# Kernel tuning notes

Measured on AMD Instinct MI355X. Metric: run time of the kernel, lower is better.

The kernel has to match this reference:

```python
import jax, jax.numpy as jnp
import numpy as np
import math

EMB_DIM = 1024
HEAD_SIZE = 64
T = 4096
B = 4

def setup_inputs() -> dict:
    key = jax.random.key(0)
    k1, k2, k3, k4 = jax.random.split(key, 4)
    scale = 1.0 / math.sqrt(EMB_DIM)
    return {
        "input": jax.random.normal(k1, (B, T, EMB_DIM), dtype=jnp.float32),
        "Wq": jax.random.normal(k2, (EMB_DIM, HEAD_SIZE), dtype=jnp.float32) * scale,
        "Wk": jax.random.normal(k3, (EMB_DIM, HEAD_SIZE), dtype=jnp.float32) * scale,
        "Wv": jax.random.normal(k4, (EMB_DIM, HEAD_SIZE), dtype=jnp.float32) * scale,
    }

def reference(input, Wq, Wk, Wv):
    # q,k,v: [B,T,H]
    q = input @ Wq
    k = input @ Wk
    v = input @ Wv
    # scores: [B,T,T]
    match = jnp.einsum('bqh,bkh->bqk', q, k)
    # 'encoder' mask in this repo = causal tril mask
    causal = jnp.tril(jnp.ones((T, T), dtype=bool))
    match = jnp.where(causal, match, -jnp.inf)
    # NOTE: faithful to source quirk: softmax first, THEN divide by sqrt(head_size)
    attention = jax.nn.softmax(match, axis=-1) / math.sqrt(HEAD_SIZE)
    return jnp.einsum('bqk,bkh->bqh', attention, v)
```

## Files before the change

### kernel.cpp

```cpp
#include <hip/hip_runtime.h>

#define T_SEQ 4096
#define NBATCH 4
#define EMB 1024
#define HS 64
#define BT (NBATCH * T_SEQ)

typedef float f32x4 __attribute__((ext_vector_type(4)));
typedef short s16x8 __attribute__((ext_vector_type(8)));

__device__ __forceinline__ unsigned short f2bf(float x) {
  union { float f; unsigned u; } c; c.f = x;
  unsigned r = c.u + 0x7FFF + ((c.u >> 16) & 1);
  return (unsigned short)(r >> 16);
}
__device__ __forceinline__ float bf2f(unsigned short h) {
  union { unsigned u; float f; } c; c.u = ((unsigned)h) << 16;
  return c.f;
}
__device__ __forceinline__ void cvt8(float4 a0, float4 a1, s16x8& hi, s16x8& lo) {
  float xv[8] = {a0.x, a0.y, a0.z, a0.w, a1.x, a1.y, a1.z, a1.w};
#pragma unroll
  for (int j = 0; j < 8; ++j) {
    unsigned short h = f2bf(xv[j]);
    hi[j] = (short)h;
    lo[j] = (short)f2bf(xv[j] - bf2f(h));
  }
}

__global__ __launch_bounds__(256) void wconv(
    const float* __restrict__ Wq, const float* __restrict__ Wk,
    const float* __restrict__ Wv, unsigned short* __restrict__ wt_hi,
    unsigned short* __restrict__ wt_lo) {
  const int n3 = blockIdx.x;
  const int which = n3 >> 6, n = n3 & 63;
  const float* W = (which == 0) ? Wq : (which == 1) ? Wk : Wv;
#pragma unroll
  for (int i = 0; i < 4; ++i) {
    int k = i * 256 + threadIdx.x;
    float x = W[(size_t)k * HS + n];
    unsigned short h = f2bf(x);
    wt_hi[(size_t)n3 * EMB + k] = h;
    wt_lo[(size_t)n3 * EMB + k] = f2bf(x - bf2f(h));
  }
}

__global__ __launch_bounds__(512) void qkv_mfma(
    const float* __restrict__ inp, const unsigned short* __restrict__ wt_hi,
    const unsigned short* __restrict__ wt_lo, float* __restrict__ qf,
    unsigned short* __restrict__ khi, unsigned short* __restrict__ klo,
    unsigned short* __restrict__ vtb) {
  __shared__ unsigned short Bhi[192 * 40];
  __shared__ unsigned short Blo[192 * 40];
  const int t = threadIdx.x, lane = t & 63, w = t >> 6;
  const int m = lane & 15, quad = lane >> 4;
  const int mg = w >> 2, ng = w & 3;
  const int tok0 = blockIdx.x * 32;
  const int arow = tok0 + mg * 16 + m;

  f32x4 acc[3];
#pragma unroll
  for (int nt = 0; nt < 3; ++nt) acc[nt] = (f32x4){0.f, 0.f, 0.f, 0.f};

  const size_t offa = (size_t)(t >> 2) * EMB + (t & 3) * 8;
  const int idxb = (t < 256) ? (t + 512) : (t - 256);
  const unsigned short* srcb = (t < 256) ? wt_hi : wt_lo;
  const size_t offb = (size_t)(idxb >> 2) * EMB + (idxb & 3) * 8;
  const int idxc = t + 256;
  const size_t offc = (size_t)(idxc >> 2) * EMB + (idxc & 3) * 8;

  uint4 bpa, bpb, bpc;
  float4 apre0, apre1;
  bpa = *(const uint4*)&wt_hi[offa];
  bpb = *(const uint4*)&srcb[offb];
  bpc = *(const uint4*)&wt_lo[offc];
  {
    const float* ap = &inp[(size_t)arow * EMB + quad * 8];
    apre0 = *(const float4*)ap;
    apre1 = *(const float4*)(ap + 4);
  }

  for (int kc = 0; kc < 32; ++kc) {
    const int k0n = (kc + 1) * 32;
    __syncthreads();
    {
      *(uint4*)&Bhi[(t >> 2) * 40 + (t & 3) * 8] = bpa;
      unsigned short* dstb = (t < 256) ? Bhi : Blo;
      *(uint4*)&dstb[(idxb >> 2) * 40 + (idxb & 3) * 8] = bpb;
      *(uint4*)&Blo[(idxc >> 2) * 40 + (idxc & 3) * 8] = bpc;
    }
    __syncthreads();

    s16x8 ah, al;
    cvt8(apre0, apre1, ah, al);

    if (kc < 31) {
      bpa = *(const uint4*)&wt_hi[offa + k0n];
      bpb = *(const uint4*)&srcb[offb + k0n];
      bpc = *(const uint4*)&wt_lo[offc + k0n];
      const float* ap = &inp[(size_t)arow * EMB + k0n + quad * 8];
      apre0 = *(const float4*)ap;
      apre1 = *(const float4*)(ap + 4);
    }

#pragma unroll
    for (int nt = 0; nt < 3; ++nt) {
      int n3 = ng * 48 + nt * 16 + m;
      s16x8 bh = *(const s16x8*)&Bhi[n3 * 40 + quad * 8];
      s16x8 bl = *(const s16x8*)&Blo[n3 * 40 + quad * 8];
      acc[nt] = __builtin_amdgcn_mfma_f32_16x16x32_bf16(ah, bh, acc[nt], 0, 0, 0);
      acc[nt] = __builtin_amdgcn_mfma_f32_16x16x32_bf16(ah, bl, acc[nt], 0, 0, 0);
      acc[nt] = __builtin_amdgcn_mfma_f32_16x16x32_bf16(al, bh, acc[nt], 0, 0, 0);
    }
  }

#pragma unroll
  for (int nt = 0; nt < 3; ++nt) {
    int n3 = ng * 48 + nt * 16 + m;
    int which = n3 >> 6, col = n3 & 63;
#pragma unroll
    for (int r = 0; r < 4; ++r) {
      int tok = tok0 + mg * 16 + quad * 4 + r;
      float val = acc[nt][r];
      if (which == 0) {
        qf[(size_t)tok * HS + col] = val;
      } else if (which == 1) {
        unsigned short h = f2bf(val);
        khi[(size_t)tok * HS + col] = h;
        klo[(size_t)tok * HS + col] = f2bf(val - bf2f(h));
      } else {
        vtb[(size_t)(tok >> 6) * 4096 + (size_t)col * 64 + (tok & 63)] = f2bf(val);
      }
    }
  }
}

__global__ __launch_bounds__(256) void attn_part(
    const float* __restrict__ q, const unsigned short* __restrict__ khi,
    const unsigned short* __restrict__ klo, const unsigned short* __restrict__ vt,
    unsigned short* __restrict__ partO, float* __restrict__ partML) {
  __shared__ unsigned short Khi_s[64 * 72];
  __shared__ unsigned short Klo_s[64 * 72];
  __shared__ unsigned short Vt_s[64 * 72];
  __shared__ unsigned short P_s[4 * 16 * 72];
  const int t = threadIdx.x;
  const int lane = t & 63, w = t >> 6;
  const int m = lane & 15, quad = lane >> 4;

  int u = blockIdx.x;
  const int b = u / 160;
  u -= b * 160;
  int qtile = 0, c = 0;
  {
    int acc2 = 0;
    for (int qq = 0; qq < 64; ++qq) {
      int ncq = (qq >> 4) + 1;
      if (u < acc2 + ncq) { qtile = qq; c = u - acc2; break; }
      acc2 += ncq;
    }
  }
  const int kt0 = c * 16;
  const int kt1 = (kt0 + 16 < qtile + 1) ? kt0 + 16 : qtile + 1;

  const size_t qrow0 = (size_t)b * T_SEQ + (size_t)qtile * 64;
  const size_t krowbase = (size_t)b * T_SEQ;
  const int q_loc = w * 16 + m;

  s16x8 qh[2], ql[2];
#pragma unroll
  for (int cc = 0; cc < 2; ++cc) {
    const float* qp = &q[(qrow0 + q_loc) * HS + cc * 32 + quad * 8];
    cvt8(*(const float4*)qp, *(const float4*)(qp + 4), qh[cc], ql[cc]);
  }

  float l_st = 0.f;
  f32x4 o[4];
#pragma unroll
  for (int hb = 0; hb < 4; ++hb) o[hb] = (f32x4){0.f, 0.f, 0.f, 0.f};

  const int r0 = t >> 3, ch0 = t & 7;
  const int r1 = (256 + t) >> 3, ch1 = t & 7;

  uint4 pk0h, pk0l, pv0, pk1h, pk1l, pv1;
  {
    size_t g0 = (krowbase + (size_t)kt0 * 64 + r0) * HS + ch0 * 8;
    size_t g1 = (krowbase + (size_t)kt0 * 64 + r1) * HS + ch1 * 8;
    pk0h = *(const uint4*)&khi[g0]; pk0l = *(const uint4*)&klo[g0];
    pk1h = *(const uint4*)&khi[g1]; pk1l = *(const uint4*)&klo[g1];
    size_t v0 = (size_t)(b * 64 + kt0) * 4096 + (size_t)r0 * 64 + ch0 * 8;
    size_t v1 = (size_t)(b * 64 + kt0) * 4096 + (size_t)r1 * 64 + ch1 * 8;
    pv0 = *(const uint4*)&vt[v0]; pv1 = *(const uint4*)&vt[v1];
  }

  for (int kt = kt0; kt < kt1; ++kt) {
    __syncthreads();
    *(uint4*)&Khi_s[r0 * 72 + ch0 * 8] = pk0h;
    *(uint4*)&Klo_s[r0 * 72 + ch0 * 8] = pk0l;
    *(uint4*)&Vt_s[r0 * 72 + ch0 * 8] = pv0;
    *(uint4*)&Khi_s[r1 * 72 + ch1 * 8] = pk1h;
    *(uint4*)&Klo_s[r1 * 72 + ch1 * 8] = pk1l;
    *(uint4*)&Vt_s[r1 * 72 + ch1 * 8] = pv1;
    __syncthreads();

    if (kt + 1 < kt1) {
      size_t g0 = (krowbase + (size_t)(kt + 1) * 64 + r0) * HS + ch0 * 8;
      size_t g1 = (krowbase + (size_t)(kt + 1) * 64 + r1) * HS + ch1 * 8;
      pk0h = *(const uint4*)&khi[g0]; pk0l = *(const uint4*)&klo[g0];
      pk1h = *(const uint4*)&khi[g1]; pk1l = *(const uint4*)&klo[g1];
      size_t v0 = (size_t)(b * 64 + kt + 1) * 4096 + (size_t)r0 * 64 + ch0 * 8;
      size_t v1 = (size_t)(b * 64 + kt + 1) * 4096 + (size_t)r1 * 64 + ch1 * 8;
      pv0 = *(const uint4*)&vt[v0]; pv1 = *(const uint4*)&vt[v1];
    }

    f32x4 st[4];
#pragma unroll
    for (int cb = 0; cb < 4; ++cb) {
      st[cb] = (f32x4){0.f, 0.f, 0.f, 0.f};
#pragma unroll
      for (int cc = 0; cc < 2; ++cc) {
        s16x8 bh = *(const s16x8*)&Khi_s[(cb * 16 + m) * 72 + cc * 32 + quad * 8];
        s16x8 bl = *(const s16x8*)&Klo_s[(cb * 16 + m) * 72 + cc * 32 + quad * 8];
        st[cb] = __builtin_amdgcn_mfma_f32_16x16x32_bf16(bh, qh[cc], st[cb], 0, 0, 0);
        st[cb] = __builtin_amdgcn_mfma_f32_16x16x32_bf16(bl, qh[cc], st[cb], 0, 0, 0);
        st[cb] = __builtin_amdgcn_mfma_f32_16x16x32_bf16(bh, ql[cc], st[cb], 0, 0, 0);
      }
    }
    if (kt == qtile) {
#pragma unroll
      for (int cb = 0; cb < 4; ++cb)
#pragma unroll
        for (int r = 0; r < 4; ++r)
          if (cb * 16 + quad * 4 + r > q_loc) st[cb][r] = -1e30f;
    }
#pragma unroll
    for (int cb = 0; cb < 4; ++cb)
#pragma unroll
      for (int r = 0; r < 4; ++r) {
        st[cb][r] = __expf(st[cb][r]);
        l_st += st[cb][r];
      }
#pragma unroll
    for (int cb = 0; cb < 4; ++cb) {
      uint2 pk;
      pk.x = (unsigned)f2bf(st[cb][0]) | ((unsigned)f2bf(st[cb][1]) << 16);
      pk.y = (unsigned)f2bf(st[cb][2]) | ((unsigned)f2bf(st[cb][3]) << 16);
      *(uint2*)&P_s[q_loc * 72 + cb * 16 + quad * 4] = pk;
    }
    s16x8 pf[2];
#pragma unroll
    for (int cc = 0; cc < 2; ++cc)
      pf[cc] = *(const s16x8*)&P_s[q_loc * 72 + cc * 32 + quad * 8];
#pragma unroll
    for (int hb = 0; hb < 4; ++hb) {
#pragma unroll
      for (int cc = 0; cc < 2; ++cc) {
        s16x8 vf = *(const s16x8*)&Vt_s[(hb * 16 + m) * 72 + cc * 32 + quad * 8];
        o[hb] = __builtin_amdgcn_mfma_f32_16x16x32_bf16(vf, pf[cc], o[hb], 0, 0, 0);
      }
    }
  }

  l_st += __shfl_xor(l_st, 16, 64);
  l_st += __shfl_xor(l_st, 32, 64);

  const int slot = ((b * 64 + qtile) << 2) + c;
  unsigned short* Op = partO + (size_t)slot * 4096;
#pragma unroll
  for (int hb = 0; hb < 4; ++hb) {
    uint2 pk;
    pk.x = (unsigned)f2bf(o[hb][0]) | ((unsigned)f2bf(o[hb][1]) << 16);
    pk.y = (unsigned)f2bf(o[hb][2]) | ((unsigned)f2bf(o[hb][3]) << 16);
    *(uint2*)&Op[q_loc * 64 + hb * 16 + quad * 4] = pk;
  }
  if (quad == 0) partML[(size_t)slot * 64 + q_loc] = l_st;
}

__global__ __launch_bounds__(256) void attn_combine(
    const unsigned short* __restrict__ partO, const float* __restrict__ partML,
    float* __restrict__ out) {
  const int qtile = blockIdx.x, b = blockIdx.y;
  const int t = threadIdx.x;
  const int row = t >> 2, hg = t & 3;
  const int nc = (qtile >> 4) + 1;
  const int slot0 = (b * 64 + qtile) << 2;

  float lsum = 0.f;
  for (int i = 0; i < nc; ++i) lsum += partML[(size_t)(slot0 + i) * 64 + row];
  const float inv = 1.f / (lsum * 8.0f);

  float acc[16];
#pragma unroll
  for (int e = 0; e < 16; ++e) acc[e] = 0.f;
  for (int i = 0; i < nc; ++i) {
    const unsigned short* Op =
        partO + (size_t)(slot0 + i) * 4096 + row * 64 + hg * 16;
    uint4 u0 = *(const uint4*)Op;
    uint4 u1 = *(const uint4*)(Op + 8);
    unsigned uv[8] = {u0.x, u0.y, u0.z, u0.w, u1.x, u1.y, u1.z, u1.w};
#pragma unroll
    for (int e = 0; e < 8; ++e) {
      acc[2 * e] += bf2f((unsigned short)(uv[e] & 0xFFFF));
      acc[2 * e + 1] += bf2f((unsigned short)(uv[e] >> 16));
    }
  }
  float* op = &out[((size_t)b * T_SEQ + (size_t)qtile * 64 + row) * HS + hg * 16];
#pragma unroll
  for (int v = 0; v < 4; ++v) {
    float4 r;
    r.x = acc[4 * v + 0] * inv; r.y = acc[4 * v + 1] * inv;
    r.z = acc[4 * v + 2] * inv; r.w = acc[4 * v + 3] * inv;
    ((float4*)op)[v] = r;
  }
}

extern "C" void kernel_launch(void* const* d_in, const int* in_sizes, int n_in,
                              void* d_out, int out_size, void* d_ws, size_t ws_size,
                              hipStream_t stream) {
  const float* inp = (const float*)d_in[0];
  const float* Wq  = (const float*)d_in[1];
  const float* Wk  = (const float*)d_in[2];
  const float* Wv  = (const float*)d_in[3];
  float* out = (float*)d_out;

  char* base = (char*)d_ws;
  float* qf = (float*)base;
  unsigned short* khi = (unsigned short*)(base + (size_t)BT * HS * 4);
  unsigned short* klo = khi + (size_t)BT * HS;
  unsigned short* vtb = klo + (size_t)BT * HS;
  unsigned short* wt_hi = vtb + (size_t)BT * HS;
  unsigned short* wt_lo = wt_hi + (size_t)192 * EMB;
  unsigned short* partO = wt_lo + (size_t)192 * EMB;
  float* partML = (float*)(partO + (size_t)1024 * 4096);

  wconv<<<dim3(192), dim3(256), 0, stream>>>(Wq, Wk, Wv, wt_hi, wt_lo);
  qkv_mfma<<<dim3(BT / 32), dim3(512), 0, stream>>>(inp, wt_hi, wt_lo, qf, khi, klo, vtb);
  attn_part<<<dim3(640), dim3(256), 0, stream>>>(qf, khi, klo, vtb, partO, partML);
  attn_combine<<<dim3(64, NBATCH), dim3(256), 0, stream>>>(partO, partML, out);
}
```

Baseline: 192.3 us.

## Enlarge QKV projection tile to 64 tokens and 64-wide K chunks

The QKV projection GEMM now processes 64 tokens per block instead of 32, with each warp computing six 16-column tiles instead of three, and walks K in chunks of 64 instead of 32. This halves the number of blocks and K-loop iterations, which cuts barrier count and how often each block reloads the shared weight tiles per token. In exchange it uses more registers per thread, more LDS per block, and launches fewer blocks (256), which may leave some CUs idle.

```diff
diff --git a/kernel.cpp b/kernel.cpp
--- a/kernel.cpp
+++ b/kernel.cpp
@@ -50,73 +50,93 @@
     const unsigned short* __restrict__ wt_lo, float* __restrict__ qf,
     unsigned short* __restrict__ khi, unsigned short* __restrict__ klo,
     unsigned short* __restrict__ vtb) {
-  __shared__ unsigned short Bhi[192 * 40];
-  __shared__ unsigned short Blo[192 * 40];
+  __shared__ unsigned short Bhi[192 * 72];
+  __shared__ unsigned short Blo[192 * 72];
   const int t = threadIdx.x, lane = t & 63, w = t >> 6;
   const int m = lane & 15, quad = lane >> 4;
-  const int mg = w >> 2, ng = w & 3;
-  const int tok0 = blockIdx.x * 32;
+  const int mg = w >> 1, ng = w & 1;
+  const int tok0 = blockIdx.x * 64;
   const int arow = tok0 + mg * 16 + m;
 
-  f32x4 acc[3];
-#pragma unroll
-  for (int nt = 0; nt < 3; ++nt) acc[nt] = (f32x4){0.f, 0.f, 0.f, 0.f};
-
-  const size_t offa = (size_t)(t >> 2) * EMB + (t & 3) * 8;
-  const int idxb = (t < 256) ? (t + 512) : (t - 256);
-  const unsigned short* srcb = (t < 256) ? wt_hi : wt_lo;
-  const size_t offb = (size_t)(idxb >> 2) * EMB + (idxb & 3) * 8;
-  const int idxc = t + 256;
-  const size_t offc = (size_t)(idxc >> 2) * EMB + (idxc & 3) * 8;
-
-  uint4 bpa, bpb, bpc;
-  float4 apre0, apre1;
-  bpa = *(const uint4*)&wt_hi[offa];
-  bpb = *(const uint4*)&srcb[offb];
-  bpc = *(const uint4*)&wt_lo[offc];
+  f32x4 acc[6];
+#pragma unroll
+  for (int nt = 0; nt < 6; ++nt) acc[nt] = (f32x4){0.f, 0.f, 0.f, 0.f};
+
+  const int s0 = t, s1 = t + 512, s2 = t + 1024;
+  const int n3_0 = s0 >> 3, k8_0 = s0 & 7;
+  const int n3_1 = s1 >> 3, k8_1 = s1 & 7;
+  const int n3_2 = s2 >> 3, k8_2 = s2 & 7;
+  const size_t goff0 = (size_t)n3_0 * EMB + k8_0 * 8;
+  const size_t goff1 = (size_t)n3_1 * EMB + k8_1 * 8;
+  const size_t goff2 = (size_t)n3_2 * EMB + k8_2 * 8;
+  const int lds0 = n3_0 * 72 + k8_0 * 8;
+  const int lds1 = n3_1 * 72 + k8_1 * 8;
+  const int lds2 = n3_2 * 72 + k8_2 * 8;
+
+  uint4 ph0, ph1, ph2, pl0, pl1, pl2;
+  float4 pa0, pa1, pa2, pa3;
+  ph0 = *(const uint4*)&wt_hi[goff0];
+  ph1 = *(const uint4*)&wt_hi[goff1];
+  ph2 = *(const uint4*)&wt_hi[goff2];
+  pl0 = *(const uint4*)&wt_lo[goff0];
+  pl1 = *(const uint4*)&wt_lo[goff1];
+  pl2 = *(const uint4*)&wt_lo[goff2];
   {
     const float* ap = &inp[(size_t)arow * EMB + quad * 8];
-    apre0 = *(const float4*)ap;
-    apre1 = *(const float4*)(ap + 4);
-  }
-
-  for (int kc = 0; kc < 32; ++kc) {
-    const int k0n = (kc + 1) * 32;
+    pa0 = *(const float4*)ap;
+    pa1 = *(const float4*)(ap + 4);
+    pa2 = *(const float4*)(ap + 32);
+    pa3 = *(const float4*)(ap + 36);
+  }
+
+  for (int kc = 0; kc < 16; ++kc) {
     __syncthreads();
-    {
-      *(uint4*)&Bhi[(t >> 2) * 40 + (t & 3) * 8] = bpa;
-      unsigned short* dstb = (t < 256) ? Bhi : Blo;
-      *(uint4*)&dstb[(idxb >> 2) * 40 + (idxb & 3) * 8] = bpb;
-      *(uint4*)&Blo[(idxc >> 2) * 40 + (idxc & 3) * 8] = bpc;
-    }
+    *(uint4*)&Bhi[lds0] = ph0;
+    *(uint4*)&Bhi[lds1] = ph1;
+    *(uint4*)&Bhi[lds2] = ph2;
+    *(uint4*)&Blo[lds0] = pl0;
+    *(uint4*)&Blo[lds1] = pl1;
+    *(uint4*)&Blo[lds2] = pl2;
     __syncthreads();
 
-    s16x8 ah, al;
-    cvt8(apre0, apre1, ah, al);
-
-    if (kc < 31) {
-      bpa = *(const uint4*)&wt_hi[offa + k0n];
-      bpb = *(const uint4*)&srcb[offb + k0n];
-      bpc = *(const uint4*)&wt_lo[offc + k0n];
+    s16x8 ah0, al0, ah1, al1;
+    cvt8(pa0, pa1, ah0, al0);
+    cvt8(pa2, pa3, ah1, al1);
+
+    if (kc < 15) {
+      const int k0n = (kc + 1) * 64;
+      ph0 = *(const uint4*)&wt_hi[goff0 + k0n];
+      ph1 = *(const uint4*)&wt_hi[goff1 + k0n];
+      ph2 = *(const uint4*)&wt_hi[goff2 + k0n];
+      pl0 = *(const uint4*)&wt_lo[goff0 + k0n];
+      pl1 = *(const uint4*)&wt_lo[goff1 + k0n];
+      pl2 = *(const uint4*)&wt_lo[goff2 + k0n];
       const float* ap = &inp[(size_t)arow * EMB + k0n + quad * 8];
-      apre0 = *(const float4*)ap;
-      apre1 = *(const float4*)(ap + 4);
-    }
-
-#pragma unroll
-    for (int nt = 0; nt < 3; ++nt) {
-      int n3 = ng * 48 + nt * 16 + m;
-      s16x8 bh = *(const s16x8*)&Bhi[n3 * 40 + quad * 8];
-      s16x8 bl = *(const s16x8*)&Blo[n3 * 40 + quad * 8];
-      acc[nt] = __builtin_amdgcn_mfma_f32_16x16x32_bf16(ah, bh, acc[nt], 0, 0, 0);
-      acc[nt] = __builtin_amdgcn_mfma_f32_16x16x32_bf16(ah, bl, acc[nt], 0, 0, 0);
-      acc[nt] = __builtin_amdgcn_mfma_f32_16x16x32_bf16(al, bh, acc[nt], 0, 0, 0);
-    }
-  }
-
-#pragma unroll
-  for (int nt = 0; nt < 3; ++nt) {
-    int n3 = ng * 48 + nt * 16 + m;
+      pa0 = *(const float4*)ap;
+      pa1 = *(const float4*)(ap + 4);
+      pa2 = *(const float4*)(ap + 32);
+      pa3 = *(const float4*)(ap + 36);
+    }
+
+#pragma unroll
+    for (int nt = 0; nt < 6; ++nt) {
+      const int n3 = ng * 96 + nt * 16 + m;
+      s16x8 bh0 = *(const s16x8*)&Bhi[n3 * 72 + quad * 8];
+      s16x8 bl0 = *(const s16x8*)&Blo[n3 * 72 + quad * 8];
+      s16x8 bh1 = *(const s16x8*)&Bhi[n3 * 72 + 32 + quad * 8];
+      s16x8 bl1 = *(const s16x8*)&Blo[n3 * 72 + 32 + quad * 8];
+      acc[nt] = __builtin_amdgcn_mfma_f32_16x16x32_bf16(ah0, bh0, acc[nt], 0, 0, 0);
+      acc[nt] = __builtin_amdgcn_mfma_f32_16x16x32_bf16(ah0, bl0, acc[nt], 0, 0, 0);
+      acc[nt] = __builtin_amdgcn_mfma_f32_16x16x32_bf16(al0, bh0, acc[nt], 0, 0, 0);
+      acc[nt] = __builtin_amdgcn_mfma_f32_16x16x32_bf16(ah1, bh1, acc[nt], 0, 0, 0);
+      acc[nt] = __builtin_amdgcn_mfma_f32_16x16x32_bf16(ah1, bl1, acc[nt], 0, 0, 0);
+      acc[nt] = __builtin_amdgcn_mfma_f32_16x16x32_bf16(al1, bh1, acc[nt], 0, 0, 0);
+    }
+  }
+
+#pragma unroll
+  for (int nt = 0; nt < 6; ++nt) {
+    int n3 = ng * 96 + nt * 16 + m;
     int which = n3 >> 6, col = n3 & 63;
 #pragma unroll
     for (int r = 0; r < 4; ++r) {
@@ -333,7 +353,7 @@
   float* partML = (float*)(partO + (size_t)1024 * 4096);
 
   wconv<<<dim3(192), dim3(256), 0, stream>>>(Wq, Wk, Wv, wt_hi, wt_lo);
-  qkv_mfma<<<dim3(BT / 32), dim3(512), 0, stream>>>(inp, wt_hi, wt_lo, qf, khi, klo, vtb);
+  qkv_mfma<<<dim3(BT / 64), dim3(512), 0, stream>>>(inp, wt_hi, wt_lo, qf, khi, klo, vtb);
   attn_part<<<dim3(640), dim3(256), 0, stream>>>(qf, khi, klo, vtb, partO, partML);
   attn_combine<<<dim3(64, NBATCH), dim3(256), 0, stream>>>(partO, partML, out);
 }
```

New measurement: 173.2 us. 9.9% less time.
